# Optimization experiments

Hardware: AMD Instinct MI355X
Metric: run time of the kernel (lower is better)

The kernel has to match this reference:

```python
import jax, jax.numpy as jnp
import numpy as np


def make_coord(h, w):
    # grid-center coords in [-1,1], stacked as (y, x), matching torch make_coord
    y = (2.0 * jnp.arange(h, dtype=jnp.float32) + 1.0) / h - 1.0
    x = (2.0 * jnp.arange(w, dtype=jnp.float32) + 1.0) / w - 1.0
    yy, xx = jnp.meshgrid(y, x, indexing='ij')
    return jnp.stack([yy, xx], axis=-1).reshape(-1, 2)  # [h*w, 2]


def setup_inputs() -> dict:
    key = jax.random.key(0)
    ks = jax.random.split(key, 11)
    N, C, Hf, Wf = 4, 64, 64, 64
    inp = {"img_feature": jax.random.normal(ks[0], (N, C, Hf, Wf), dtype=jnp.float32)}
    dims = [68, 256, 256, 256, 256, 3]  # in_dim = C + 2 (rel_coord) + 2 (rel_cell)
    for i in range(5):
        inp[f"w{i}"] = jax.random.normal(ks[1 + i], (dims[i], dims[i + 1]), dtype=jnp.float32) * (1.0 / np.sqrt(dims[i]))
        inp[f"b{i}"] = jax.random.normal(ks[6 + i], (dims[i + 1],), dtype=jnp.float32) * 0.01
    inp["h"] = 256
    inp["w"] = 256
    inp["cell_scale"] = 1
    inp["bsize"] = 30000
    return inp


def _forward(img_feature, w0, b0, w1, b1, w2, b2, w3, b3, w4, b4, h, w, cell_scale):
    feat = img_feature
    N, C, Hf, Wf = feat.shape
    Q = h * w
    coord = make_coord(h, w)  # [Q, 2] (y, x)
    cell = jnp.stack([
        jnp.full((Q,), 2.0 / (h * cell_scale), dtype=jnp.float32),
        jnp.full((Q,), 2.0 / (w * cell_scale), dtype=jnp.float32),
    ], axis=-1)  # [Q, 2]

    rx = 1.0 / Hf  # = 2 / Hf / 2
    ry = 1.0 / Wf
    eps_shift = 1e-6
    scale = jnp.array([Hf, Wf], dtype=jnp.float32)
    rel_cell = cell * scale  # [Q, 2]

    # features laid out for per-query gather: [N, Hf*Wf, C]
    feat_flat = jnp.transpose(feat, (0, 2, 3, 1)).reshape(N, Hf * Wf, C)

    layers = [(w0, b0), (w1, b1), (w2, b2), (w3, b3), (w4, b4)]

    def mlp(x):
        for wi, bi in layers[:-1]:
            x = jax.nn.relu(x @ wi + bi)
        wl, bl = layers[-1]
        return x @ wl + bl

    preds = []
    areas = []
    for vx in (-1, 1):
        for vy in (-1, 1):
            c = coord + jnp.array([vx * rx + eps_shift, vy * ry + eps_shift], dtype=jnp.float32)
            c = jnp.clip(c, -1.0 + 1e-6, 1.0 - 1e-6)
            # grid_sample nearest, align_corners=False: idx = round(((g+1)*S - 1)/2)
            iy = jnp.clip(jnp.round(((c[:, 0] + 1.0) * Hf - 1.0) * 0.5), 0, Hf - 1).astype(jnp.int32)
            ix = jnp.clip(jnp.round(((c[:, 1] + 1.0) * Wf - 1.0) * 0.5), 0, Wf - 1).astype(jnp.int32)
            idx = iy * Wf + ix  # [Q]
            q_feat = feat_flat[:, idx, :]  # [N, Q, C] irregular gather
            # nearest feature-grid center coords (same values grid_sample of feat_coord returns)
            q_coord = jnp.stack([
                (2.0 * iy.astype(jnp.float32) + 1.0) / Hf - 1.0,
                (2.0 * ix.astype(jnp.float32) + 1.0) / Wf - 1.0,
            ], axis=-1)  # [Q, 2]
            rel = (coord - q_coord) * scale  # [Q, 2]
            x = jnp.concatenate([
                q_feat,
                jnp.broadcast_to(rel[None], (N, Q, 2)),
                jnp.broadcast_to(rel_cell[None], (N, Q, 2)),
            ], axis=-1)  # [N, Q, 68]
            preds.append(mlp(x))  # [N, Q, 3]
            areas.append(jnp.abs(rel[:, 0] * rel[:, 1]) + 1e-9)  # [Q]

    tot_area = areas[0] + areas[1] + areas[2] + areas[3]
    # local-ensemble swap: 0<->3, 1<->2 (opposite-corner weighting)
    areas = [areas[3], areas[2], areas[1], areas[0]]
    ret = jnp.zeros((N, Q, 3), dtype=jnp.float32)
    for p, a in zip(preds, areas):
        ret = ret + p * (a / tot_area)[None, :, None]
    return jnp.transpose(ret.reshape(N, h, w, 3), (0, 3, 1, 2))  # [N, 3, h, w]


def reference(img_feature, w0, b0, w1, b1, w2, b2, w3, b3, w4, b4, h, w, cell_scale, bsize):
    # bsize only chunks the query loop in the original; math is identical without chunking
    return _forward(img_feature, w0, b0, w1, b1, w2, b2, w3, b3, w4, b4, h, w, cell_scale)
```

## Files before the change

kernel.cpp:

```cpp
#include <hip/hip_runtime.h>


typedef _Float16 f16;
typedef _Float16 f16x8 __attribute__((ext_vector_type(8)));
typedef _Float16 f16x4 __attribute__((ext_vector_type(4)));
typedef float    f32x4 __attribute__((ext_vector_type(4)));

#define MFMA(a, b, c) __builtin_amdgcn_mfma_f32_16x16x32_f16((a), (b), (c), 0, 0, 0)

constexpr int HF = 64, WF = 64;
constexpr int HO = 256, WO = 256;
constexpr int Q = HO * WO;
constexpr int D = 256;
constexpr int K0P = 96;
constexpr int STR = 264;
constexpr int R = 128;

constexpr size_t OFF_FEAT = 0;
constexpr size_t OFF_W0   = 2097152;
constexpr size_t OFF_W1   = OFF_W0 + 256 * 96 * 2;
constexpr size_t OFF_W2   = OFF_W1 + 256 * 256 * 2;
constexpr size_t OFF_W3   = OFF_W2 + 256 * 256 * 2;
constexpr size_t OFF_W4   = OFF_W3 + 256 * 256 * 2;

__global__ void prep_feat(const float* __restrict__ f, f16* __restrict__ ft) {
  int idx = blockIdx.x * 256 + threadIdx.x;
  int c = idx & 63, p = (idx >> 6) & 4095, n = idx >> 18;
  ft[idx] = (f16)f[((((size_t)n << 6) | c) << 12) | p];
}

__global__ void prep_w(const float* __restrict__ w, f16* __restrict__ wt,
                       int K, int N, int Kpad, int Npad) {
  int idx = blockIdx.x * 256 + threadIdx.x;
  if (idx >= Npad * Kpad) return;
  int k = idx % Kpad, n = idx / Kpad;
  wt[idx] = (f16)((k < K && n < N) ? w[k * N + n] : 0.0f);
}

__device__ __forceinline__ void tap_geom(int q, float vx, float vy,
                                         int& p, float& rel0, float& rel1) {
  int qy = q >> 8, qx = q & (WO - 1);
  float cy0 = (float)(2 * qy + 1) * (1.0f / HO) - 1.0f;
  float cx0 = (float)(2 * qx + 1) * (1.0f / WO) - 1.0f;
  float cy = cy0 + vx * (1.0f / HF) + 1e-6f;
  float cx = cx0 + vy * (1.0f / WF) + 1e-6f;
  cy = fminf(fmaxf(cy, -1.0f + 1e-6f), 1.0f - 1e-6f);
  cx = fminf(fmaxf(cx, -1.0f + 1e-6f), 1.0f - 1e-6f);
  int iy = (int)rintf(((cy + 1.0f) * (float)HF - 1.0f) * 0.5f);
  int ix = (int)rintf(((cx + 1.0f) * (float)WF - 1.0f) * 0.5f);
  iy = min(max(iy, 0), HF - 1);
  ix = min(max(ix, 0), WF - 1);
  p = (iy << 6) | ix;
  rel0 = (cy0 - ((float)(2 * iy + 1) * (1.0f / HF) - 1.0f)) * (float)HF;
  rel1 = (cx0 - ((float)(2 * ix + 1) * (1.0f / WF) - 1.0f)) * (float)WF;
}

__device__ __forceinline__ float blend_wt(int q, int t) {
  float a[4], tot = 0.0f;
#pragma unroll
  for (int u = 0; u < 4; ++u) {
    int p; float r0, r1;
    tap_geom(q, (u & 2) ? 1.0f : -1.0f, (u & 1) ? 1.0f : -1.0f, p, r0, r1);
    a[u] = fabsf(r0 * r1) + 1e-9f;
    tot += a[u];
  }
  float sel = (t == 0) ? a[3] : (t == 1) ? a[2] : (t == 2) ? a[1] : a[0];
  return sel / tot;
}

template <int KSTEPS, int KPAD>
__device__ __forceinline__ void mlp_layer(f16* X, const f16* __restrict__ wt,
                                          const float* __restrict__ bv,
                                          int wv, int col, int quad) {
  f32x4 acc[4][8];
#pragma unroll
  for (int mt = 0; mt < 4; ++mt)
#pragma unroll
    for (int nt = 0; nt < 8; ++nt) acc[mt][nt] = 0.0f;

  const f16* ap = wt + (wv * 64 + col) * KPAD + quad * 8;
  const f16* bp = X + col * STR + quad * 8;
#pragma unroll 1
  for (int s = 0; s < KSTEPS; ++s) {
    f16x8 b[8];
#pragma unroll
    for (int nt = 0; nt < 8; ++nt)
      b[nt] = *(const f16x8*)(bp + s * 32 + nt * 16 * STR);
#pragma unroll
    for (int mt = 0; mt < 4; ++mt) {
      f16x8 a = *(const f16x8*)(ap + s * 32 + mt * 16 * KPAD);
#pragma unroll
      for (int nt = 0; nt < 8; ++nt) acc[mt][nt] = MFMA(a, b[nt], acc[mt][nt]);
    }
  }
  __syncthreads();
#pragma unroll
  for (int mt = 0; mt < 4; ++mt) {
    float4 bb = *(const float4*)(bv + wv * 64 + mt * 16 + quad * 4);
#pragma unroll
    for (int nt = 0; nt < 8; ++nt) {
      f16x4 y;
      y[0] = (f16)fmaxf(acc[mt][nt][0] + bb.x, 0.0f);
      y[1] = (f16)fmaxf(acc[mt][nt][1] + bb.y, 0.0f);
      y[2] = (f16)fmaxf(acc[mt][nt][2] + bb.z, 0.0f);
      y[3] = (f16)fmaxf(acc[mt][nt][3] + bb.w, 0.0f);
      *(f16x4*)(X + (nt * 16 + col) * STR + wv * 64 + mt * 16 + quad * 4) = y;
    }
  }
  __syncthreads();
}

__global__ __launch_bounds__(256, 2) void liif_main(
    const f16* __restrict__ featT,
    const f16* __restrict__ wt0, const f16* __restrict__ wt1,
    const f16* __restrict__ wt2, const f16* __restrict__ wt3,
    const f16* __restrict__ wt4,
    const float* __restrict__ b0, const float* __restrict__ b1,
    const float* __restrict__ b2, const float* __restrict__ b3,
    const float* __restrict__ b4, float* __restrict__ out) {
  __shared__ __attribute__((aligned(16))) f16 X[R * STR];
  const int tid = threadIdx.x;
  const int wv = tid >> 6;
  const int lane = tid & 63;
  const int row0 = blockIdx.x * R;
  const int n = row0 >> 16;
  const int q0 = row0 & (Q - 1);
  const int col = lane & 15, quad = lane >> 4;

  float oacc[2][4] = {{0, 0, 0, 0}, {0, 0, 0, 0}};
  float bias4[4];
#pragma unroll
  for (int i = 0; i < 4; ++i) bias4[i] = (i < 3) ? b4[i] : 0.0f;

#pragma unroll 1
  for (int t = 0; t < 4; ++t) {
    const float vx = (t & 2) ? 1.0f : -1.0f;
    const float vy = (t & 1) ? 1.0f : -1.0f;

    __syncthreads();
    {
      const int gr = tid >> 1, hf = tid & 1;
      int p; float r0, r1;
      tap_geom(q0 + gr, vx, vy, p, r0, r1);
      const f16x8* src = (const f16x8*)(featT + (((size_t)n << 12) + p) * 64 + hf * 32);
      f16x8* dst = (f16x8*)(X + gr * STR + hf * 32);
      dst[0] = src[0]; dst[1] = src[1]; dst[2] = src[2]; dst[3] = src[3];
      if (tid < R) {
        int p2; float s0, s1;
        tap_geom(q0 + tid, vx, vy, p2, s0, s1);
        f16* xr = X + tid * STR;
        f16x4 relv = {(f16)s0, (f16)s1, (f16)0.5f, (f16)0.5f};
        *(f16x4*)(xr + 64) = relv;
        f16x4 z4 = {0, 0, 0, 0};
        f16x8 z8 = {0, 0, 0, 0, 0, 0, 0, 0};
        *(f16x4*)(xr + 68) = z4;
        *(f16x8*)(xr + 72) = z8;
        *(f16x8*)(xr + 80) = z8;
        *(f16x8*)(xr + 88) = z8;
      }
    }
    __syncthreads();

    mlp_layer<3, K0P>(X, wt0, b0, wv, col, quad);
    mlp_layer<8, D>(X, wt1, b1, wv, col, quad);
    mlp_layer<8, D>(X, wt2, b2, wv, col, quad);
    mlp_layer<8, D>(X, wt3, b3, wv, col, quad);

    f32x4 facc[2];
    facc[0] = 0.0f; facc[1] = 0.0f;
    {
      const f16* ap = wt4 + col * D + quad * 8;
      const f16* bp = X + (wv * 32 + col) * STR + quad * 8;
#pragma unroll 1
      for (int s = 0; s < 8; ++s) {
        f16x8 a = *(const f16x8*)(ap + s * 32);
        f16x8 bq0 = *(const f16x8*)(bp + s * 32);
        f16x8 bq1 = *(const f16x8*)(bp + 16 * STR + s * 32);
        facc[0] = MFMA(a, bq0, facc[0]);
        facc[1] = MFMA(a, bq1, facc[1]);
      }
    }
#pragma unroll
    for (int nt = 0; nt < 2; ++nt) {
      int q = q0 + wv * 32 + nt * 16 + col;
      float w = blend_wt(q, t);
#pragma unroll
      for (int i = 0; i < 4; ++i) oacc[nt][i] += (facc[nt][i] + bias4[i]) * w;
    }
  }

  if (quad == 0) {
#pragma unroll
    for (int nt = 0; nt < 2; ++nt) {
      int q = q0 + wv * 32 + nt * 16 + col;
#pragma unroll
      for (int c = 0; c < 3; ++c)
        out[(((size_t)(n * 3 + c)) << 16) + q] = oacc[nt][c];
    }
  }
}

extern "C" void kernel_launch(void* const* d_in, const int* in_sizes, int n_in,
                              void* d_out, int out_size, void* d_ws, size_t ws_size,
                              hipStream_t stream) {
  const float* feat = (const float*)d_in[0];
  const float* w0 = (const float*)d_in[1];
  const float* b0 = (const float*)d_in[2];
  const float* w1 = (const float*)d_in[3];
  const float* b1 = (const float*)d_in[4];
  const float* w2 = (const float*)d_in[5];
  const float* b2 = (const float*)d_in[6];
  const float* w3 = (const float*)d_in[7];
  const float* b3 = (const float*)d_in[8];
  const float* w4 = (const float*)d_in[9];
  const float* b4 = (const float*)d_in[10];

  char* ws = (char*)d_ws;
  f16* featT = (f16*)(ws + OFF_FEAT);
  f16* wt0 = (f16*)(ws + OFF_W0);
  f16* wt1 = (f16*)(ws + OFF_W1);
  f16* wt2 = (f16*)(ws + OFF_W2);
  f16* wt3 = (f16*)(ws + OFF_W3);
  f16* wt4 = (f16*)(ws + OFF_W4);

  prep_feat<<<4096, 256, 0, stream>>>(feat, featT);
  prep_w<<<(256 * 96 + 255) / 256, 256, 0, stream>>>(w0, wt0, 68, 256, 96, 256);
  prep_w<<<256, 256, 0, stream>>>(w1, wt1, 256, 256, 256, 256);
  prep_w<<<256, 256, 0, stream>>>(w2, wt2, 256, 256, 256, 256);
  prep_w<<<256, 256, 0, stream>>>(w3, wt3, 256, 256, 256, 256);
  prep_w<<<(16 * 256 + 255) / 256, 256, 0, stream>>>(w4, wt4, 256, 3, 256, 16);

  liif_main<<<Q * 4 / R, 256, 0, stream>>>(featT, wt0, wt1, wt2, wt3, wt4,
                                           b0, b1, b2, b3, b4, (float*)d_out);
}
```

Measured before the change: 617.9 us.

## Split each block's MLP work across eight waves instead of four

Block size doubles to 512 threads, and each wave now computes 32 output features per layer instead of 64, cutting accumulator registers in half. The final layer and output use 16 rows per wave, and the gather uses four threads per row. The aim is more resident waves per CU to hide LDS and global latency. In exchange, each wave gets less reuse of B-fragments loaded from LDS, so LDS read traffic per MFMA goes up.

```diff
diff --git a/kernel.cpp b/kernel.cpp
--- a/kernel.cpp
+++ b/kernel.cpp
@@ -72,31 +72,37 @@
 __device__ __forceinline__ void mlp_layer(f16* X, const f16* __restrict__ wt,
                                           const float* __restrict__ bv,
                                           int wv, int col, int quad) {
-  f32x4 acc[4][8];
-#pragma unroll
-  for (int mt = 0; mt < 4; ++mt)
+  f32x4 acc[2][8];
+#pragma unroll
+  for (int mt = 0; mt < 2; ++mt)
 #pragma unroll
     for (int nt = 0; nt < 8; ++nt) acc[mt][nt] = 0.0f;
 
-  const f16* ap = wt + (wv * 64 + col) * KPAD + quad * 8;
+  const f16* ap = wt + (wv * 32 + col) * KPAD + quad * 8;
   const f16* bp = X + col * STR + quad * 8;
+
 #pragma unroll 1
   for (int s = 0; s < KSTEPS; ++s) {
-    f16x8 b[8];
-#pragma unroll
-    for (int nt = 0; nt < 8; ++nt)
-      b[nt] = *(const f16x8*)(bp + s * 32 + nt * 16 * STR);
-#pragma unroll
-    for (int mt = 0; mt < 4; ++mt) {
-      f16x8 a = *(const f16x8*)(ap + s * 32 + mt * 16 * KPAD);
-#pragma unroll
-      for (int nt = 0; nt < 8; ++nt) acc[mt][nt] = MFMA(a, b[nt], acc[mt][nt]);
-    }
-  }
+    f16x8 a0 = *(const f16x8*)(ap + s * 32);
+    f16x8 a1 = *(const f16x8*)(ap + s * 32 + 16 * KPAD);
+#pragma unroll
+    for (int half = 0; half < 2; ++half) {
+      f16x8 b[4];
+#pragma unroll
+      for (int nt = 0; nt < 4; ++nt)
+        b[nt] = *(const f16x8*)(bp + s * 32 + (half * 4 + nt) * 16 * STR);
+#pragma unroll
+      for (int nt = 0; nt < 4; ++nt) {
+        acc[0][half * 4 + nt] = MFMA(a0, b[nt], acc[0][half * 4 + nt]);
+        acc[1][half * 4 + nt] = MFMA(a1, b[nt], acc[1][half * 4 + nt]);
+      }
+    }
+  }
+
   __syncthreads();
 #pragma unroll
-  for (int mt = 0; mt < 4; ++mt) {
-    float4 bb = *(const float4*)(bv + wv * 64 + mt * 16 + quad * 4);
+  for (int mt = 0; mt < 2; ++mt) {
+    float4 bb = *(const float4*)(bv + wv * 32 + mt * 16 + quad * 4);
 #pragma unroll
     for (int nt = 0; nt < 8; ++nt) {
       f16x4 y;
@@ -104,13 +110,13 @@
       y[1] = (f16)fmaxf(acc[mt][nt][1] + bb.y, 0.0f);
       y[2] = (f16)fmaxf(acc[mt][nt][2] + bb.z, 0.0f);
       y[3] = (f16)fmaxf(acc[mt][nt][3] + bb.w, 0.0f);
-      *(f16x4*)(X + (nt * 16 + col) * STR + wv * 64 + mt * 16 + quad * 4) = y;
+      *(f16x4*)(X + (nt * 16 + col) * STR + wv * 32 + mt * 16 + quad * 4) = y;
     }
   }
   __syncthreads();
 }
 
-__global__ __launch_bounds__(256, 2) void liif_main(
+__global__ __launch_bounds__(512, 4) void liif_main(
     const f16* __restrict__ featT,
     const f16* __restrict__ wt0, const f16* __restrict__ wt1,
     const f16* __restrict__ wt2, const f16* __restrict__ wt3,
@@ -127,7 +133,7 @@
   const int q0 = row0 & (Q - 1);
   const int col = lane & 15, quad = lane >> 4;
 
-  float oacc[2][4] = {{0, 0, 0, 0}, {0, 0, 0, 0}};
+  float oacc[4] = {0, 0, 0, 0};
   float bias4[4];
 #pragma unroll
   for (int i = 0; i < 4; ++i) bias4[i] = (i < 3) ? b4[i] : 0.0f;
@@ -139,12 +145,12 @@
 
     __syncthreads();
     {
-      const int gr = tid >> 1, hf = tid & 1;
+      const int gr = tid >> 2, part = tid & 3;
       int p; float r0, r1;
       tap_geom(q0 + gr, vx, vy, p, r0, r1);
-      const f16x8* src = (const f16x8*)(featT + (((size_t)n << 12) + p) * 64 + hf * 32);
-      f16x8* dst = (f16x8*)(X + gr * STR + hf * 32);
-      dst[0] = src[0]; dst[1] = src[1]; dst[2] = src[2]; dst[3] = src[3];
+      const f16x8* src = (const f16x8*)(featT + (((size_t)n << 12) + p) * 64) + part * 2;
+      f16x8* dst = (f16x8*)(X + gr * STR) + part * 2;
+      dst[0] = src[0]; dst[1] = src[1];
       if (tid < R) {
         int p2; float s0, s1;
         tap_geom(q0 + tid, vx, vy, p2, s0, s1);
@@ -166,37 +172,30 @@
     mlp_layer<8, D>(X, wt2, b2, wv, col, quad);
     mlp_layer<8, D>(X, wt3, b3, wv, col, quad);
 
-    f32x4 facc[2];
-    facc[0] = 0.0f; facc[1] = 0.0f;
+    f32x4 facc = 0.0f;
     {
       const f16* ap = wt4 + col * D + quad * 8;
-      const f16* bp = X + (wv * 32 + col) * STR + quad * 8;
+      const f16* bp = X + (wv * 16 + col) * STR + quad * 8;
 #pragma unroll 1
       for (int s = 0; s < 8; ++s) {
         f16x8 a = *(const f16x8*)(ap + s * 32);
-        f16x8 bq0 = *(const f16x8*)(bp + s * 32);
-        f16x8 bq1 = *(const f16x8*)(bp + 16 * STR + s * 32);
-        facc[0] = MFMA(a, bq0, facc[0]);
-        facc[1] = MFMA(a, bq1, facc[1]);
+        f16x8 b = *(const f16x8*)(bp + s * 32);
+        facc = MFMA(a, b, facc);
       }
     }
-#pragma unroll
-    for (int nt = 0; nt < 2; ++nt) {
-      int q = q0 + wv * 32 + nt * 16 + col;
+    {
+      int q = q0 + wv * 16 + col;
       float w = blend_wt(q, t);
 #pragma unroll
-      for (int i = 0; i < 4; ++i) oacc[nt][i] += (facc[nt][i] + bias4[i]) * w;
+      for (int i = 0; i < 4; ++i) oacc[i] += (facc[i] + bias4[i]) * w;
     }
   }
 
   if (quad == 0) {
-#pragma unroll
-    for (int nt = 0; nt < 2; ++nt) {
-      int q = q0 + wv * 32 + nt * 16 + col;
-#pragma unroll
-      for (int c = 0; c < 3; ++c)
-        out[(((size_t)(n * 3 + c)) << 16) + q] = oacc[nt][c];
-    }
+    int q = q0 + wv * 16 + col;
+#pragma unroll
+    for (int c = 0; c < 3; ++c)
+      out[(((size_t)(n * 3 + c)) << 16) + q] = oacc[c];
   }
 }
 
@@ -230,6 +229,6 @@
   prep_w<<<256, 256, 0, stream>>>(w3, wt3, 256, 256, 256, 256);
   prep_w<<<(16 * 256 + 255) / 256, 256, 0, stream>>>(w4, wt4, 256, 3, 256, 16);
 
-  liif_main<<<Q * 4 / R, 256, 0, stream>>>(featT, wt0, wt1, wt2, wt3, wt4,
+  liif_main<<<Q * 4 / R, 512, 0, stream>>>(featT, wt0, wt1, wt2, wt3, wt4,
                                            b0, b1, b2, b3, b4, (float*)d_out);
 }
```

After: 631.8 us. 2.2% more time.
